# Kernel tuning notes

Hardware: AMD Instinct MI355X
Metric: run time of the kernel (lower is better)

The kernel has to match this reference:

```python
import jax, jax.numpy as jnp
import numpy as np

S_MUL, V_MUL = 32, 16          # 32x0e + 16x1o
NODE_DIM = S_MUL + 3 * V_MUL   # 80
LATENT = 128
INV_SQRT3 = 1.0 / np.sqrt(3.0)          # wigner 3j (1,1,0) / (0,1,1) / (1,0,1) factor
C_SCALAR = np.float32(1.0 / np.sqrt(48.0))   # path_norm 'element': fan into 0e = 32*1 + 16*1
C_VECTOR = np.float32(np.sqrt(3.0 / 48.0))   # irrep dim 3 / fan 48 for 1o output


def setup_inputs() -> dict:
    rng = np.random.default_rng(0)
    B, n_atoms, radius = 2048, 32, 5.0
    N = B * n_atoms
    # atoms uniform in a 10A cube -> ~300 edges per 32-atom graph at r=5
    pos_g = rng.uniform(0.0, 10.0, size=(B, n_atoms, 3)).astype(np.float32)
    diff = pos_g[:, :, None, :] - pos_g[:, None, :, :]
    d2 = (diff * diff).sum(-1)
    mask = (d2 <= radius * radius) & (d2 > 0.0)   # same predicate as build_radius_graph
    b_idx, i_idx, j_idx = np.nonzero(mask)
    edge_index = np.stack([b_idx * n_atoms + i_idx, b_idx * n_atoms + j_idx]).astype(np.int32)
    pos = pos_g.reshape(N, 3)
    z = rng.integers(0, 100, size=N).astype(np.int32)
    batch = np.repeat(np.arange(B, dtype=np.int32), n_atoms)
    L = 3  # num_layers

    def w(*shape, scale=1.0):
        return jnp.asarray((rng.standard_normal(shape) * scale).astype(np.float32))

    return dict(
        pos=jnp.asarray(pos), z=jnp.asarray(z), batch=jnp.asarray(batch),
        edge_index=jnp.asarray(edge_index), num_graphs=B,
        emb=w(100, S_MUL),                      # nn.Embedding(100, 32) ~ N(0,1)
        W_s2n=w(S_MUL, S_MUL),                  # e3nn Linear 32x0e -> 32x0e path
        W1=w(L, S_MUL, S_MUL),                  # tp path 0e x 0e -> 0e
        W2=w(L, S_MUL, V_MUL),                  # tp path 0e x 1o -> 1o
        W3=w(L, V_MUL, V_MUL),                  # tp path 1o x 0e -> 1o
        W4=w(L, V_MUL, S_MUL),                  # tp path 1o x 1o -> 0e
        Ws=w(L, S_MUL, S_MUL),                  # e3nn Linear scalar block
        Wv=w(L, V_MUL, V_MUL),                  # e3nn Linear vector block
        Wr1=w(NODE_DIM, 256, scale=1.0 / np.sqrt(NODE_DIM)), br1=jnp.zeros((256,), jnp.float32),
        Wr2=w(256, LATENT, scale=1.0 / np.sqrt(256.0)), br2=jnp.zeros((LATENT,), jnp.float32),
    )


def _forward(pos, emb, W_s2n, W1, W2, W3, W4, Ws, Wv, Wr1, br1, Wr2, br2,
             z, batch, edge_index, num_graphs):
    N = pos.shape[0]
    src, dst = edge_index[0], edge_index[1]
    # atom embedding -> node irreps (only 0e->0e path exists; vectors start at 0)
    s = (emb[z] @ W_s2n) * np.float32(1.0 / np.sqrt(S_MUL))   # (N, 32)
    v = jnp.zeros((N, V_MUL, 3), pos.dtype)                   # (N, 16, 3)
    # spherical harmonics, normalize=True, 'component': Y0 = 1, Y1 = sqrt(3) * r_hat
    rij = pos[dst] - pos[src]                                 # (E, 3)
    sh1 = np.float32(np.sqrt(3.0)) * rij / jnp.linalg.norm(rij, axis=-1, keepdims=True)
    for l in range(W1.shape[0]):
        ss, vs = s[src], v[src]                               # gather (E,32), (E,16,3)
        # FullyConnectedTensorProduct(node, sh, node), uvw weights, sh0 == 1
        m_s = C_SCALAR * (jnp.einsum('eu,uw->ew', ss, W1[l])
                          + INV_SQRT3 * jnp.einsum('eui,ei,uw->ew', vs, sh1, W4[l]))
        m_v = (C_VECTOR * INV_SQRT3) * (jnp.einsum('eu,ei,uw->ewi', ss, sh1, W2[l])
                                        + jnp.einsum('eui,uw->ewi', vs, W3[l]))
        a_s = jax.ops.segment_sum(m_s, dst, num_segments=N)   # index_add_ scatter
        a_v = jax.ops.segment_sum(m_v, dst, num_segments=N)
        # e3nn Linear (per-irrep block, 1/sqrt(fan_in)) then relu on FULL feature (as in source)
        h_s = jax.nn.relu((a_s @ Ws[l]) * np.float32(1.0 / np.sqrt(S_MUL)))
        h_v = jax.nn.relu(jnp.einsum('nvi,vw->nwi', a_v, Wv[l]) * np.float32(1.0 / np.sqrt(V_MUL)))
        s, v = s + h_s, v + h_v                               # residual
    x = jnp.concatenate([s, v.reshape(N, V_MUL * 3)], axis=-1)  # (N, 80)
    hg = jax.ops.segment_sum(x, batch, num_segments=num_graphs) # sum-pool per graph
    return jax.nn.relu(hg @ Wr1 + br1) @ Wr2 + br2              # (B, latent)


def reference(pos, emb, W_s2n, W1, W2, W3, W4, Ws, Wv, Wr1, br1, Wr2, br2,
              z, batch, edge_index, num_graphs):
    return _forward(pos, emb, W_s2n, W1, W2, W3, W4, Ws, Wv, Wr1, br1, Wr2, br2,
                    z, batch, edge_index, num_graphs)
```

## Files before the change

kernel.cpp:

```cpp
#include <hip/hip_runtime.h>
#include <math.h>

typedef __attribute__((ext_vector_type(8))) short bf16x8;
typedef __attribute__((ext_vector_type(4))) float f32x4;

#define SQRT3F     1.7320508075688772f
#define SCALE_T    0.17677669529663687f
#define SCALE_M1   0.025515518153991442f
#define SCALE_M2   0.014731391274719739f
#define SCALE_M34  0.036084391824351615f

#define FSTR 40

__device__ __forceinline__ ushort f2bf(float f) {
    union { float f; unsigned u; } v; v.f = f;
    unsigned u = v.u;
    return (ushort)((u + 0x7FFFu + ((u >> 16) & 1u)) >> 16);
}
__device__ __forceinline__ float bf2f(ushort h) {
    union { unsigned u; float f; } v; v.u = ((unsigned)h) << 16;
    return v.f;
}
__device__ __forceinline__ unsigned cvtpk(float lo, float hi) {
    unsigned r;
    asm("v_cvt_pk_bf16_f32 %0, %1, %2" : "=v"(r) : "v"(lo), "v"(hi));
    return r;
}
__device__ __forceinline__ void pl32(unsigned &a, unsigned &b) {
    auto r = __builtin_amdgcn_permlane32_swap(a, b, false, false);
    a = r[0]; b = r[1];
}
__device__ __forceinline__ void pl16(unsigned &a, unsigned &b) {
    auto r = __builtin_amdgcn_permlane16_swap(a, b, false, false);
    a = r[0]; b = r[1];
}
__device__ __forceinline__ f32x4 mfma(bf16x8 a, bf16x8 b, f32x4 c) {
    return __builtin_amdgcn_mfma_f32_16x16x32_bf16(a, b, c, 0, 0, 0);
}
__device__ __forceinline__ bf16x8 makeFrag(f32x4 T0, f32x4 T1) {
    unsigned p0 = cvtpk(T0[0], T0[1]), p1 = cvtpk(T0[2], T0[3]);
    unsigned q0 = cvtpk(T1[0], T1[1]), q1 = cvtpk(T1[2], T1[3]);
    pl32(p0, q0); pl16(p0, q0);
    pl32(p1, q1); pl16(p1, q1);
    union { bf16x8 v; unsigned u[4]; } r;
    r.u[0] = p0; r.u[1] = p1; r.u[2] = q0; r.u[3] = q1;
    return r.v;
}
__device__ __forceinline__ bf16x8 makeFragZ(f32x4 T2) {
    unsigned s0 = cvtpk(T2[0], T2[1]), s1 = cvtpk(T2[2], T2[3]);
    unsigned z0 = 0u, z1 = 0u;
    pl32(s0, z0); pl16(s0, z0);
    pl32(s1, z1); pl16(s1, z1);
    union { bf16x8 v; unsigned u[4]; } r;
    r.u[0] = s0; r.u[1] = s1; r.u[2] = z0; r.u[3] = z1;
    return r.v;
}
__device__ __forceinline__ void accRelu(f32x4 &S, f32x4 h) {
    S[0] += fmaxf(h[0], 0.f); S[1] += fmaxf(h[1], 0.f);
    S[2] += fmaxf(h[2], 0.f); S[3] += fmaxf(h[3], 0.f);
}

__global__ void prep_kernel(const float* __restrict__ emb,
                            const float* __restrict__ W_s2n,
                            const float* __restrict__ W1, const float* __restrict__ W2,
                            const float* __restrict__ W3, const float* __restrict__ W4,
                            const float* __restrict__ Ws, const float* __restrict__ Wv,
                            ushort* __restrict__ Tbf, ushort* __restrict__ Mbf)
{
    int idx = blockIdx.x * blockDim.x + threadIdx.x;
    if (idx < 3200) {
        int r = idx >> 5, c = idx & 31;
        float acc = 0.f;
        for (int k = 0; k < 32; ++k) acc += emb[r*32 + k] * W_s2n[k*32 + c];
        Tbf[idx] = f2bf(acc * SCALE_T);
        return;
    }
    idx -= 3200;
    if (idx < 3*48*64) {
        int lyr = idx / 3072, rem = idx % 3072;
        int row = rem >> 6, u = rem & 63;
        float val = 0.f;
        if (row < 32) {
            int w = row;
            if (u < 32) {
                float a = 0.f;
                for (int k = 0; k < 32; ++k)
                    a += W1[lyr*1024 + u*32 + k] * Ws[lyr*1024 + k*32 + w];
                val = a * SCALE_M1;
            } else if (u < 48) {
                int uu = u - 32; float a = 0.f;
                for (int k = 0; k < 32; ++k)
                    a += W4[lyr*512 + uu*32 + k] * Ws[lyr*1024 + k*32 + w];
                val = a * SCALE_M2;
            }
        } else {
            int w = row - 32;
            if (u < 32) {
                float a = 0.f;
                for (int k = 0; k < 16; ++k)
                    a += W2[lyr*512 + u*16 + k] * Wv[lyr*256 + k*16 + w];
                val = a * SCALE_M34;
            } else if (u < 48) {
                int uu = u - 32; float a = 0.f;
                for (int k = 0; k < 16; ++k)
                    a += W3[lyr*256 + uu*16 + k] * Wv[lyr*256 + k*16 + w];
                val = a * SCALE_M34;
            }
        }
        Mbf[lyr*3072 + row*64 + u] = f2bf(val);
    }
}

__global__ __launch_bounds__(256)
void gnn_kernel(const float* __restrict__ pos, const int* __restrict__ z,
                const ushort* __restrict__ Tbf, const ushort* __restrict__ Mbf,
                const float* __restrict__ Wr1, const float* __restrict__ br1,
                const float* __restrict__ Wr2, const float* __restrict__ br2,
                float* __restrict__ out, int B)
{
    __shared__ __align__(16) char smem[26880];
    ushort* featA = (ushort*)smem;
    float*  hgl   = (float*)(smem + 25600);
    float*  h1    = (float*)smem;
    float*  red   = (float*)(smem + 4096);

    const int tid = threadIdx.x;
    const int wv = tid >> 6, l = tid & 63;
    const int g  = blockIdx.x*4 + wv;
    ushort* F  = featA + wv*80*FSTR;
    const int ln = l & 15, kq = l >> 4;

    {
        int n = l & 31, h = l >> 5;
        int zg = z[g*32 + n];
        uint4 t0 = *(const uint4*)(Tbf + zg*32 + h*16);
        uint4 t1 = *(const uint4*)(Tbf + zg*32 + h*16 + 8);
        unsigned ua[8] = {t0.x, t0.y, t0.z, t0.w, t1.x, t1.y, t1.z, t1.w};
        #pragma unroll
        for (int q = 0; q < 8; ++q) {
            F[(h*16 + 2*q    )*FSTR + n] = (ushort)ua[q];
            F[(h*16 + 2*q + 1)*FSTR + n] = (ushort)(ua[q] >> 16);
        }
    }

    f32x4 Ss[2][2];
    f32x4 Sv[2][3];
    #pragma unroll
    for (int mt = 0; mt < 2; ++mt) {
        #pragma unroll
        for (int wt = 0; wt < 2; ++wt) {
            uint2 d = *(const uint2*)&F[(wt*16 + ln)*FSTR + mt*16 + kq*4];
            Ss[mt][wt][0] = bf2f((ushort)(d.x      ));
            Ss[mt][wt][1] = bf2f((ushort)(d.x >> 16));
            Ss[mt][wt][2] = bf2f((ushort)(d.y      ));
            Ss[mt][wt][3] = bf2f((ushort)(d.y >> 16));
        }
        #pragma unroll
        for (int i = 0; i < 3; ++i)
            Sv[mt][i] = (f32x4){0.f, 0.f, 0.f, 0.f};
    }

    bf16x8 adjf[4][2];
    {
        const int k0 = kq*8;
        #pragma unroll
        for (int nt = 0; nt < 2; ++nt) {
            int ng = g*32 + nt*16 + ln;
            float px = pos[3*ng], py = pos[3*ng+1], pz = pos[3*ng+2];
            union { bf16x8 v; ushort s[8]; } o[4];
            #pragma unroll
            for (int jj = 0; jj < 8; ++jj) {
                int j = g*32 + k0 + jj;
                float dx = __fsub_rn(px, pos[3*j]);
                float dy = __fsub_rn(py, pos[3*j+1]);
                float dz = __fsub_rn(pz, pos[3*j+2]);
                float d2 = __fadd_rn(__fadd_rn(__fmul_rn(dx,dx), __fmul_rn(dy,dy)),
                                     __fmul_rn(dz,dz));
                bool on = (d2 <= 25.0f) && (d2 > 0.0f);
                float rinv = on ? rsqrtf(d2) * SQRT3F : 0.f;
                o[0].s[jj] = on ? (ushort)0x3F80 : (ushort)0;
                o[1].s[jj] = f2bf(dx * rinv);
                o[2].s[jj] = f2bf(dy * rinv);
                o[3].s[jj] = f2bf(dz * rinv);
            }
            #pragma unroll
            for (int w = 0; w < 4; ++w) adjf[w][nt] = o[w].v;
        }
    }

    const f32x4 z4 = {0.f, 0.f, 0.f, 0.f};

    for (int lay = 0; lay < 3; ++lay) {
        const ushort* Mg = Mbf + lay*3072;
        bf16x8 fs0 = makeFrag(Ss[0][0], Ss[1][0]);
        bf16x8 fs1 = makeFrag(Ss[0][1], Ss[1][1]);
        bf16x8 fv0 = makeFrag(Sv[0][0], Sv[1][0]);
        bf16x8 fv1 = makeFrag(Sv[0][1], Sv[1][1]);
        bf16x8 fv2 = makeFrag(Sv[0][2], Sv[1][2]);
        bf16x8 bmS0[2], bmS1[2], bmV[2];
        #pragma unroll
        for (int kc = 0; kc < 2; ++kc) {
            bmS0[kc] = *(const bf16x8*)&Mg[(     ln)*64 + kc*32 + kq*8];
            bmS1[kc] = *(const bf16x8*)&Mg[(16 + ln)*64 + kc*32 + kq*8];
            bmV [kc] = *(const bf16x8*)&Mg[(32 + ln)*64 + kc*32 + kq*8];
        }

        bf16x8 agf[2][2];

        #pragma unroll
        for (int nt = 0; nt < 2; ++nt) {
            f32x4 T0 = mfma(fs0, adjf[0][nt], z4);
            f32x4 T1 = mfma(fs1, adjf[0][nt], z4);
            f32x4 T2 = mfma(fv2, adjf[3][nt], z4);
            T2 = mfma(fv1, adjf[2][nt], T2);
            T2 = mfma(fv0, adjf[1][nt], T2);
            agf[nt][0] = makeFrag(T0, T1);
            agf[nt][1] = makeFragZ(T2);
        }
        f32x4 hs[2][2] = {{z4, z4}, {z4, z4}};
        #pragma unroll
        for (int kc = 0; kc < 2; ++kc)
            #pragma unroll
            for (int mt = 0; mt < 2; ++mt) {
                hs[mt][0] = mfma(agf[mt][kc], bmS0[kc], hs[mt][0]);
                hs[mt][1] = mfma(agf[mt][kc], bmS1[kc], hs[mt][1]);
            }
        #pragma unroll
        for (int mt = 0; mt < 2; ++mt)
            #pragma unroll
            for (int wt = 0; wt < 2; ++wt)
                accRelu(Ss[mt][wt], hs[mt][wt]);

        #pragma unroll
        for (int i = 0; i < 3; ++i) {
            bf16x8 fvi = (i == 0) ? fv0 : (i == 1) ? fv1 : fv2;
            #pragma unroll
            for (int nt = 0; nt < 2; ++nt) {
                f32x4 T0 = mfma(fs0, adjf[1+i][nt], z4);
                f32x4 T1 = mfma(fs1, adjf[1+i][nt], z4);
                f32x4 T2 = mfma(fvi, adjf[0][nt], z4);
                agf[nt][0] = makeFrag(T0, T1);
                agf[nt][1] = makeFragZ(T2);
            }
            f32x4 hv[2] = {z4, z4};
            #pragma unroll
            for (int kc = 0; kc < 2; ++kc)
                #pragma unroll
                for (int mt = 0; mt < 2; ++mt)
                    hv[mt] = mfma(agf[mt][kc], bmV[kc], hv[mt]);
            #pragma unroll
            for (int mt = 0; mt < 2; ++mt)
                accRelu(Sv[mt][i], hv[mt]);
        }
    }

    #pragma unroll
    for (int mt = 0; mt < 2; ++mt) {
        #pragma unroll
        for (int wt = 0; wt < 2; ++wt) {
            uint2 w;
            w.x = cvtpk(Ss[mt][wt][0], Ss[mt][wt][1]);
            w.y = cvtpk(Ss[mt][wt][2], Ss[mt][wt][3]);
            *(uint2*)&F[(wt*16 + ln)*FSTR + mt*16 + kq*4] = w;
        }
        #pragma unroll
        for (int i = 0; i < 3; ++i) {
            uint2 w;
            w.x = cvtpk(Sv[mt][i][0], Sv[mt][i][1]);
            w.y = cvtpk(Sv[mt][i][2], Sv[mt][i][3]);
            *(uint2*)&F[(32 + i*16 + ln)*FSTR + mt*16 + kq*4] = w;
        }
    }

    for (int f = l; f < 80; f += 64) {
        const ushort* row;
        if (f < 32) row = &F[f*FSTR];
        else { int c = f - 32, w = c/3, i = c - 3*w; row = &F[(32 + i*16 + w)*FSTR]; }
        const uint* r32 = (const uint*)row;
        float acc = 0.f;
        #pragma unroll
        for (int q = 0; q < 16; ++q) {
            uint u = r32[q];
            acc += bf2f((ushort)u) + bf2f((ushort)(u >> 16));
        }
        hgl[wv*80 + f] = acc;
    }
    __syncthreads();

    {
        const int w = tid;
        float acc0 = br1[w];
        float acc1 = acc0, acc2 = acc0, acc3 = acc0;
        #pragma unroll 4
        for (int f = 0; f < 80; ++f) {
            float wvv = Wr1[f*256 + w];
            acc0 = fmaf(hgl[0*80 + f], wvv, acc0);
            acc1 = fmaf(hgl[1*80 + f], wvv, acc1);
            acc2 = fmaf(hgl[2*80 + f], wvv, acc2);
            acc3 = fmaf(hgl[3*80 + f], wvv, acc3);
        }
        h1[0*256 + w] = fmaxf(acc0, 0.f);
        h1[1*256 + w] = fmaxf(acc1, 0.f);
        h1[2*256 + w] = fmaxf(acc2, 0.f);
        h1[3*256 + w] = fmaxf(acc3, 0.f);
    }
    __syncthreads();
    {
        const int g0 = blockIdx.x * 4;
        const int w2 = tid & 127, kh = tid >> 7;
        const float4* h1v = (const float4*)h1;
        float s0 = 0.f, s1 = 0.f, s2 = 0.f, s3 = 0.f;
        #pragma unroll 2
        for (int k4 = kh*32; k4 < kh*32 + 32; ++k4) {
            float4 hA = h1v[0*64 + k4];
            float4 hB = h1v[1*64 + k4];
            float4 hC = h1v[2*64 + k4];
            float4 hD = h1v[3*64 + k4];
            int k = k4 * 4;
            float m0 = Wr2[(size_t)(k+0)*128 + w2];
            float m1 = Wr2[(size_t)(k+1)*128 + w2];
            float m2 = Wr2[(size_t)(k+2)*128 + w2];
            float m3 = Wr2[(size_t)(k+3)*128 + w2];
            s0 = fmaf(hA.x,m0, fmaf(hA.y,m1, fmaf(hA.z,m2, fmaf(hA.w,m3, s0))));
            s1 = fmaf(hB.x,m0, fmaf(hB.y,m1, fmaf(hB.z,m2, fmaf(hB.w,m3, s1))));
            s2 = fmaf(hC.x,m0, fmaf(hC.y,m1, fmaf(hC.z,m2, fmaf(hC.w,m3, s2))));
            s3 = fmaf(hD.x,m0, fmaf(hD.y,m1, fmaf(hD.z,m2, fmaf(hD.w,m3, s3))));
        }
        if (kh) {
            red[0*128 + w2] = s0; red[1*128 + w2] = s1;
            red[2*128 + w2] = s2; red[3*128 + w2] = s3;
        }
        __syncthreads();
        if (!kh) {
            float b = br2[w2];
            out[(size_t)(g0+0)*128 + w2] = s0 + red[0*128 + w2] + b;
            out[(size_t)(g0+1)*128 + w2] = s1 + red[1*128 + w2] + b;
            out[(size_t)(g0+2)*128 + w2] = s2 + red[2*128 + w2] + b;
            out[(size_t)(g0+3)*128 + w2] = s3 + red[3*128 + w2] + b;
        }
    }
}

extern "C" void kernel_launch(void* const* d_in, const int* in_sizes, int n_in,
                              void* d_out, int out_size, void* d_ws, size_t ws_size,
                              hipStream_t stream)
{
    const float* pos   = (const float*)d_in[0];
    const int*   z     = (const int*)d_in[1];
    const float* emb   = (const float*)d_in[5];
    const float* W_s2n = (const float*)d_in[6];
    const float* W1    = (const float*)d_in[7];
    const float* W2    = (const float*)d_in[8];
    const float* W3    = (const float*)d_in[9];
    const float* W4    = (const float*)d_in[10];
    const float* Ws    = (const float*)d_in[11];
    const float* Wv    = (const float*)d_in[12];
    const float* Wr1   = (const float*)d_in[13];
    const float* br1   = (const float*)d_in[14];
    const float* Wr2   = (const float*)d_in[15];
    const float* br2   = (const float*)d_in[16];
    float* out = (float*)d_out;

    const int B = out_size / 128;

    char* p = (char*)d_ws;
    ushort* Tbf = (ushort*)p;  p += 6400;
    ushort* Mbf = (ushort*)p;  p += 18432;

    const int prep_total = 3200 + 3*48*64;
    prep_kernel<<<(prep_total + 255) / 256, 256, 0, stream>>>(
        emb, W_s2n, W1, W2, W3, W4, Ws, Wv, Tbf, Mbf);

    gnn_kernel<<<B / 4, 256, 0, stream>>>(pos, z, Tbf, Mbf,
                                          Wr1, br1, Wr2, br2, out, B);
}
```

Before: 110.3 us.

## Permute MFMA K ordering to drop permlane swaps in fragment conversion

Reorders the K index used by the MFMA operands: the fused weight matrix is stored in a permuted column order and the adjacency fragments sample neighbours in a matching interleaved order. The f32 accumulator output can then be packed straight into the bf16 A-operand layout, with no permlane32/permlane16 swaps. This removes lane-shuffle instructions from the dependent chain between chained MFMAs. In exchange it adds inline asm with an s_nop 3 per conversion to cover the MFMA-result read hazard, and correctness depends on the permutation matching on both sides.

New measurement: 109.9 us, median of 2. Within noise of the previous version (-0.4%).

```diff
diff --git a/kernel.cpp b/kernel.cpp
--- a/kernel.cpp
+++ b/kernel.cpp
@@ -26,33 +26,29 @@
     asm("v_cvt_pk_bf16_f32 %0, %1, %2" : "=v"(r) : "v"(lo), "v"(hi));
     return r;
 }
-__device__ __forceinline__ void pl32(unsigned &a, unsigned &b) {
-    auto r = __builtin_amdgcn_permlane32_swap(a, b, false, false);
-    a = r[0]; b = r[1];
-}
-__device__ __forceinline__ void pl16(unsigned &a, unsigned &b) {
-    auto r = __builtin_amdgcn_permlane16_swap(a, b, false, false);
-    a = r[0]; b = r[1];
-}
 __device__ __forceinline__ f32x4 mfma(bf16x8 a, bf16x8 b, f32x4 c) {
     return __builtin_amdgcn_mfma_f32_16x16x32_bf16(a, b, c, 0, 0, 0);
 }
-__device__ __forceinline__ bf16x8 makeFrag(f32x4 T0, f32x4 T1) {
-    unsigned p0 = cvtpk(T0[0], T0[1]), p1 = cvtpk(T0[2], T0[3]);
-    unsigned q0 = cvtpk(T1[0], T1[1]), q1 = cvtpk(T1[2], T1[3]);
-    pl32(p0, q0); pl16(p0, q0);
-    pl32(p1, q1); pl16(p1, q1);
+__device__ __forceinline__ bf16x8 frag2(f32x4 A, f32x4 B) {
     union { bf16x8 v; unsigned u[4]; } r;
-    r.u[0] = p0; r.u[1] = p1; r.u[2] = q0; r.u[3] = q1;
+    asm("v_cvt_pk_bf16_f32 %0, %4, %5\n\t"
+        "v_cvt_pk_bf16_f32 %1, %6, %7\n\t"
+        "v_cvt_pk_bf16_f32 %2, %8, %9\n\t"
+        "v_cvt_pk_bf16_f32 %3, %10, %11\n\t"
+        "s_nop 3"
+        : "=&v"(r.u[0]), "=&v"(r.u[1]), "=&v"(r.u[2]), "=&v"(r.u[3])
+        : "v"(A[0]), "v"(A[1]), "v"(A[2]), "v"(A[3]),
+          "v"(B[0]), "v"(B[1]), "v"(B[2]), "v"(B[3]));
     return r.v;
 }
-__device__ __forceinline__ bf16x8 makeFragZ(f32x4 T2) {
-    unsigned s0 = cvtpk(T2[0], T2[1]), s1 = cvtpk(T2[2], T2[3]);
-    unsigned z0 = 0u, z1 = 0u;
-    pl32(s0, z0); pl16(s0, z0);
-    pl32(s1, z1); pl16(s1, z1);
+__device__ __forceinline__ bf16x8 frag1z(f32x4 A) {
     union { bf16x8 v; unsigned u[4]; } r;
-    r.u[0] = s0; r.u[1] = s1; r.u[2] = z0; r.u[3] = z1;
+    asm("v_cvt_pk_bf16_f32 %0, %2, %3\n\t"
+        "v_cvt_pk_bf16_f32 %1, %4, %5\n\t"
+        "s_nop 3"
+        : "=&v"(r.u[0]), "=&v"(r.u[1])
+        : "v"(A[0]), "v"(A[1]), "v"(A[2]), "v"(A[3]));
+    r.u[2] = 0u; r.u[3] = 0u;
     return r.v;
 }
 __device__ __forceinline__ void accRelu(f32x4 &S, f32x4 h) {
@@ -78,7 +74,9 @@
     idx -= 3200;
     if (idx < 3*48*64) {
         int lyr = idx / 3072, rem = idx % 3072;
-        int row = rem >> 6, u = rem & 63;
+        int row = rem >> 6, c = rem & 63;
+        int kc = c >> 5, c5 = c & 31, kq2 = c5 >> 3, e = c5 & 7;
+        int u = kc*32 + (e >> 2)*16 + kq2*4 + (e & 3);
         float val = 0.f;
         if (row < 32) {
             int w = row;
@@ -107,7 +105,7 @@
                 val = a * SCALE_M34;
             }
         }
-        Mbf[lyr*3072 + row*64 + u] = f2bf(val);
+        Mbf[lyr*3072 + row*64 + c] = f2bf(val);
     }
 }
 
@@ -162,7 +160,6 @@
 
     bf16x8 adjf[4][2];
     {
-        const int k0 = kq*8;
         #pragma unroll
         for (int nt = 0; nt < 2; ++nt) {
             int ng = g*32 + nt*16 + ln;
@@ -170,7 +167,7 @@
             union { bf16x8 v; ushort s[8]; } o[4];
             #pragma unroll
             for (int jj = 0; jj < 8; ++jj) {
-                int j = g*32 + k0 + jj;
+                int j = g*32 + ((jj >> 2) << 4) + kq*4 + (jj & 3);
                 float dx = __fsub_rn(px, pos[3*j]);
                 float dy = __fsub_rn(py, pos[3*j+1]);
                 float dz = __fsub_rn(pz, pos[3*j+2]);
@@ -192,11 +189,11 @@
 
     for (int lay = 0; lay < 3; ++lay) {
         const ushort* Mg = Mbf + lay*3072;
-        bf16x8 fs0 = makeFrag(Ss[0][0], Ss[1][0]);
-        bf16x8 fs1 = makeFrag(Ss[0][1], Ss[1][1]);
-        bf16x8 fv0 = makeFrag(Sv[0][0], Sv[1][0]);
-        bf16x8 fv1 = makeFrag(Sv[0][1], Sv[1][1]);
-        bf16x8 fv2 = makeFrag(Sv[0][2], Sv[1][2]);
+        bf16x8 fs0 = frag2(Ss[0][0], Ss[1][0]);
+        bf16x8 fs1 = frag2(Ss[0][1], Ss[1][1]);
+        bf16x8 fv0 = frag2(Sv[0][0], Sv[1][0]);
+        bf16x8 fv1 = frag2(Sv[0][1], Sv[1][1]);
+        bf16x8 fv2 = frag2(Sv[0][2], Sv[1][2]);
         bf16x8 bmS0[2], bmS1[2], bmV[2];
         #pragma unroll
         for (int kc = 0; kc < 2; ++kc) {
@@ -214,8 +211,8 @@
             f32x4 T2 = mfma(fv2, adjf[3][nt], z4);
             T2 = mfma(fv1, adjf[2][nt], T2);
             T2 = mfma(fv0, adjf[1][nt], T2);
-            agf[nt][0] = makeFrag(T0, T1);
-            agf[nt][1] = makeFragZ(T2);
+            agf[nt][0] = frag2(T0, T1);
+            agf[nt][1] = frag1z(T2);
         }
         f32x4 hs[2][2] = {{z4, z4}, {z4, z4}};
         #pragma unroll
@@ -239,8 +236,8 @@
                 f32x4 T0 = mfma(fs0, adjf[1+i][nt], z4);
                 f32x4 T1 = mfma(fs1, adjf[1+i][nt], z4);
                 f32x4 T2 = mfma(fvi, adjf[0][nt], z4);
-                agf[nt][0] = makeFrag(T0, T1);
-                agf[nt][1] = makeFragZ(T2);
+                agf[nt][0] = frag2(T0, T1);
+                agf[nt][1] = frag1z(T2);
             }
             f32x4 hv[2] = {z4, z4};
             #pragma unroll
```
